# Performance work log

Hardware: AMD Instinct MI355X
Metric: run time of the kernel (lower is better)

## Reference

```python
import jax, jax.numpy as jnp
import numpy as np

B, T, V, D, U = 256, 1024, 6, 64, 64  # batch, seq, vocab, embed dim, lstm units


def _lstm_dir(x_seq, mask_seq, Wk, Wr, b, reverse):
    # x_seq: [B,T,D], mask_seq: [B,T] bool. Keras gate order: i, f, g(cell), o.
    Bc, Tc, _ = x_seq.shape
    Uc = Wr.shape[0]
    if reverse:
        x_seq = x_seq[:, ::-1, :]
        mask_seq = mask_seq[:, ::-1]
    # precompute input projections for all timesteps (one big GEMM)
    xproj = jnp.einsum('btd,dg->tbg', x_seq, Wk) + b          # [T,B,4U]
    m = jnp.swapaxes(mask_seq, 0, 1)[..., None]               # [T,B,1]

    def step(carry, inp):
        h, c = carry
        xp, mt = inp
        z = xp + h @ Wr                                        # [B,4U]
        i, f, g, o = jnp.split(z, 4, axis=-1)
        i = jax.nn.sigmoid(i)
        f = jax.nn.sigmoid(f)
        g = jnp.tanh(g)
        o = jax.nn.sigmoid(o)
        c_new = f * c + i * g
        h_new = o * jnp.tanh(c_new)
        # masked steps carry state through and repeat previous output
        h = jnp.where(mt, h_new, h)
        c = jnp.where(mt, c_new, c)
        return (h, c), h

    h0 = jnp.zeros((Bc, Uc), x_seq.dtype)
    _, ys = jax.lax.scan(step, (h0, h0), (xproj, m))           # ys: [T,B,U]
    ys = jnp.swapaxes(ys, 0, 1)                                # [B,T,U]
    if reverse:
        ys = ys[:, ::-1, :]
    return ys


def reference(tokens, emb, Wk_f, Wr_f, b_f, Wk_b, Wr_b, b_b, Wd, bd):
    x = emb[tokens]                                            # [B,T,D]
    mask = jnp.any(x != 0, axis=-1)                            # Masking(0): all-zero feature vec -> masked
    y_f = _lstm_dir(x, mask, Wk_f, Wr_f, b_f, reverse=False)   # [B,T,U]
    y_b = _lstm_dir(x, mask, Wk_b, Wr_b, b_b, reverse=True)    # [B,T,U]
    y = jnp.concatenate([y_f, y_b], axis=-1)                   # [B,T,2U]
    last = y[:, -1, :]                                         # [B,2U]
    return last @ Wd + bd                                      # [B,1]


def setup_inputs() -> dict:
    key = jax.random.key(0)
    ks = jax.random.split(key, 8)
    return {
        'tokens': jax.random.randint(ks[0], (B, T), 0, V, dtype=jnp.int32),
        'emb': jax.random.normal(ks[1], (V, D), dtype=jnp.float32),
        'Wk_f': jax.random.normal(ks[2], (D, 4 * U), dtype=jnp.float32) * 0.05,
        'Wr_f': jax.random.normal(ks[3], (U, 4 * U), dtype=jnp.float32) * 0.05,
        'b_f': jnp.zeros((4 * U,), dtype=jnp.float32),
        'Wk_b': jax.random.normal(ks[4], (D, 4 * U), dtype=jnp.float32) * 0.05,
        'Wr_b': jax.random.normal(ks[5], (U, 4 * U), dtype=jnp.float32) * 0.05,
        'b_b': jnp.zeros((4 * U,), dtype=jnp.float32),
        'Wd': jax.random.normal(ks[6], (2 * U, 1), dtype=jnp.float32) * 0.05,
        'bd': jnp.zeros((1,), dtype=jnp.float32),
    }
```

## Files before the change

kernel.cpp:

```cpp
#include <hip/hip_runtime.h>


constexpr int kB = 256;
constexpr int kT = 1024;
constexpr int kV = 6;
constexpr int kD = 64;
constexpr int kU = 64;
constexpr int kG = 256;

#define LOG2E 1.44269504f

typedef _Float16 v2h __attribute__((ext_vector_type(2)));

template <int CTRL>
__device__ __forceinline__ float dppf(float x) {
    return __int_as_float(
        __builtin_amdgcn_mov_dpp(__float_as_int(x), CTRL, 0xF, 0xF, true));
}
constexpr int kXor1 = 0xB1;
constexpr int kXor2 = 0x4E;
constexpr int kBc0 = 0x00, kBc1 = 0x55, kBc2 = 0xAA, kBc3 = 0xFF;

__device__ __forceinline__ float fast_rcp(float x) { return __builtin_amdgcn_rcpf(x); }
__device__ __forceinline__ float exp2_f(float x)   { return __builtin_amdgcn_exp2f(x); }
__device__ __forceinline__ float tanh_f(float z) { return 2.0f * fast_rcp(1.0f + exp2_f(-2.0f * LOG2E * z)) - 1.0f; }

__device__ __forceinline__ v2h as_v2h(float x) { return __builtin_bit_cast(v2h, x); }

__global__ __launch_bounds__(256)
__attribute__((amdgpu_waves_per_eu(1, 1)))
void bilstm_last_kernel(
    const int*   __restrict__ tokens,
    const float* __restrict__ emb,
    const float* __restrict__ Wk_f,
    const float* __restrict__ Wr_f,
    const float* __restrict__ b_f,
    const float* __restrict__ Wk_b,
    const float* __restrict__ b_b,
    const float* __restrict__ Wd,
    const float* __restrict__ bd,
    float*       __restrict__ out)
{
    __shared__ float s_emb[kV * kD];
    __shared__ int   __align__(16) s_tok[kT];
    __shared__ _Float16 __align__(16) s_hh[2][kU];
    __shared__ float s_red[4];

    const int b   = blockIdx.x;
    const int tid = threadIdx.x;
    const int l   = tid & 63;
    const int wv  = tid >> 6;
    const int s   = l & 3;
    const int k   = l >> 2;
    const int u   = wv * 16 + k;
    const int col = s * kU + u;

    for (int i = tid; i < kV * kD; i += 256) s_emb[i] = emb[i];
    ((int4*)s_tok)[tid] = ((const int4*)(tokens + b * kT))[tid];
    if (tid < 2 * kU) ((_Float16*)s_hh)[tid] = (_Float16)0.f;
    __syncthreads();

    unsigned int mbv = 0;
#pragma unroll
    for (int v = 0; v < kV; ++v) {
        const unsigned long long bb = __ballot(s_emb[v * kD + l] != 0.0f);
        mbv |= (bb != 0ull) ? (1u << v) : 0u;
    }
    const unsigned int smb = __builtin_amdgcn_readfirstlane(mbv);

    const int tokL = __builtin_amdgcn_readfirstlane(s_tok[kT - 1]);

    const bool  isg    = (s == 2);
    const float aScale = isg ? -2.0f * LOG2E : -LOG2E;
    const float aMul   = isg ? 2.0f : 1.0f;
    const float aAdd   = isg ? -1.0f : 0.0f;

    float pf0, pf1, pf2, pf3, pf4, pf5;
    float ab;
    {
        float afv[kV];
        const float bf = b_f[col];
#pragma unroll
        for (int v = 0; v < kV; ++v) afv[v] = bf;
        ab = b_b[col];
#pragma unroll 4
        for (int d = 0; d < kD; ++d) {
            const float wkf = Wk_f[d * kG + col];
            const float wkb = Wk_b[d * kG + col];
            afv[0] = fmaf(s_emb[0 * kD + d], wkf, afv[0]);
            afv[1] = fmaf(s_emb[1 * kD + d], wkf, afv[1]);
            afv[2] = fmaf(s_emb[2 * kD + d], wkf, afv[2]);
            afv[3] = fmaf(s_emb[3 * kD + d], wkf, afv[3]);
            afv[4] = fmaf(s_emb[4 * kD + d], wkf, afv[4]);
            afv[5] = fmaf(s_emb[5 * kD + d], wkf, afv[5]);
            ab     = fmaf(s_emb[tokL * kD + d], wkb, ab);
        }
        pf0 = afv[0]; pf1 = afv[1]; pf2 = afv[2];
        pf3 = afv[3]; pf4 = afv[4]; pf5 = afv[5];
    }
    auto sel6 = [&](int t) -> float {
        return t == 0 ? pf0 : t == 1 ? pf1 : t == 2 ? pf2
             : t == 3 ? pf3 : t == 4 ? pf4 : pf5;
    };

    float hb_val;
    {
        const float e = exp2_f(ab * aScale);
        const float r = fast_rcp(1.0f + e);
        const float a = fmaf(r, aMul, aAdd);
        const float cb = dppf<kBc0>(a) * dppf<kBc2>(a);
        const float hb = dppf<kBc3>(a) * tanh_f(cb);
        hb_val = ((smb >> tokL) & 1) ? hb : 0.0f;
    }

#define DECLH(g, p)                                                           \
    v2h wh##g##_##p;                                                          \
    wh##g##_##p.x = (_Float16)Wr_f[(16 * s + 2 * (p) + 0) * kG + ((g) * 64 + u)]; \
    wh##g##_##p.y = (_Float16)Wr_f[(16 * s + 2 * (p) + 1) * kG + ((g) * 64 + u)];
    DECLH(0,0) DECLH(0,1) DECLH(0,2) DECLH(0,3) DECLH(0,4) DECLH(0,5) DECLH(0,6) DECLH(0,7)
    DECLH(1,0) DECLH(1,1) DECLH(1,2) DECLH(1,3) DECLH(1,4) DECLH(1,5) DECLH(1,6) DECLH(1,7)
    DECLH(2,0) DECLH(2,1) DECLH(2,2) DECLH(2,3) DECLH(2,4) DECLH(2,5) DECLH(2,6) DECLH(2,7)
    DECLH(3,0) DECLH(3,1) DECLH(3,2) DECLH(3,3) DECLH(3,4) DECLH(3,5) DECLH(3,6) DECLH(3,7)
#undef DECLH

    float c = 0.0f, hreg = 0.0f;

    int st0 = __builtin_amdgcn_readfirstlane(s_tok[0]);
    int st1 = __builtin_amdgcn_readfirstlane(s_tok[1]);
    int st2 = __builtin_amdgcn_readfirstlane(s_tok[2]);
    int st3 = __builtin_amdgcn_readfirstlane(s_tok[3]);
    float zc0 = sel6(st0), zc1 = sel6(st1);
    int   mk0 = (smb >> st0) & 1, mk1 = (smb >> st1) & 1;

#define DOTG(g)                                                               \
        float pa##g = __builtin_amdgcn_fdot2(H0, wh##g##_0, 0.0f, false);     \
        float pb##g = __builtin_amdgcn_fdot2(H1, wh##g##_1, 0.0f, false);     \
        pa##g = __builtin_amdgcn_fdot2(H2, wh##g##_2, pa##g, false);          \
        pb##g = __builtin_amdgcn_fdot2(H3, wh##g##_3, pb##g, false);          \
        pa##g = __builtin_amdgcn_fdot2(H4, wh##g##_4, pa##g, false);          \
        pb##g = __builtin_amdgcn_fdot2(H5, wh##g##_5, pb##g, false);          \
        pa##g = __builtin_amdgcn_fdot2(H6, wh##g##_6, pa##g, false);          \
        pb##g = __builtin_amdgcn_fdot2(H7, wh##g##_7, pb##g, false);          \
        float p##g = pa##g + pb##g;

#define STEP(RP, WP, ZC, MK)                                                  \
    {                                                                         \
           \
        const float4* hp = (const float4*)s_hh[RP];                           \
        const float4 hv0 = hp[s * 2 + 0];                                     \
        const float4 hv1 = hp[s * 2 + 1];                                     \
        const v2h H0 = as_v2h(hv0.x), H1 = as_v2h(hv0.y);                     \
        const v2h H2 = as_v2h(hv0.z), H3 = as_v2h(hv0.w);                     \
        const v2h H4 = as_v2h(hv1.x), H5 = as_v2h(hv1.y);                     \
        const v2h H6 = as_v2h(hv1.z), H7 = as_v2h(hv1.w);                     \
        DOTG(0) DOTG(1) DOTG(2) DOTG(3)                                       \
            \
        p0 += dppf<kXor1>(p0); p1 += dppf<kXor1>(p1);                         \
        p2 += dppf<kXor1>(p2); p3 += dppf<kXor1>(p3);                         \
        float X = (s & 1) ? p1 : p0;                                          \
        float Y = (s & 1) ? p3 : p2;                                          \
        X += dppf<kXor2>(X); Y += dppf<kXor2>(Y);                             \
        const float z = ((s & 2) ? Y : X) + (ZC);                             \
                                      \
        const float e = exp2_f(z * aScale);                                   \
        const float r = fast_rcp(1.0f + e);                                   \
        const float a = fmaf(r, aMul, aAdd);                                  \
                     \
        const float ai = dppf<kBc0>(a);                                       \
        const float af = dppf<kBc1>(a);                                       \
        const float ag = dppf<kBc2>(a);                                       \
        const float ao = dppf<kBc3>(a);                                       \
        const float cn = fmaf(af, c, ai * ag);                                \
        const float hn = ao * tanh_f(cn);                                     \
        if (MK) { c = cn; hreg = hn; }                    \
        if (s == 0) s_hh[WP][u] = (_Float16)hreg;                             \
        __syncthreads();                                                      \
    }

#pragma unroll 1
    for (int t = 0; t < kT; t += 2) {
        STEP(0, 1, zc0, mk0)
        const int2 vt = *((const int2*)(s_tok + ((t + 4) & (kT - 1))));
        const float zn0 = sel6(st2); const int mn0 = (smb >> st2) & 1;
        const float zn1 = sel6(st3); const int mn1 = (smb >> st3) & 1;
        STEP(1, 0, zc1, mk1)
        st2 = __builtin_amdgcn_readfirstlane(vt.x);
        st3 = __builtin_amdgcn_readfirstlane(vt.y);
        zc0 = zn0; zc1 = zn1; mk0 = mn0; mk1 = mn1;
    }
#undef STEP
#undef DOTG

    {
        float v = (s == 0) ? (hreg * Wd[u] + hb_val * Wd[kU + u]) : 0.0f;
#pragma unroll
        for (int off = 32; off > 0; off >>= 1) v += __shfl_down(v, off, 64);
        if (l == 0) s_red[wv] = v;
    }
    __syncthreads();
    if (tid == 0) out[b] = (s_red[0] + s_red[1]) + (s_red[2] + s_red[3]) + bd[0];
}

extern "C" void kernel_launch(void* const* d_in, const int* in_sizes, int n_in,
                              void* d_out, int out_size, void* d_ws, size_t ws_size,
                              hipStream_t stream) {
    const int*   tokens = (const int*)d_in[0];
    const float* emb    = (const float*)d_in[1];
    const float* Wk_f   = (const float*)d_in[2];
    const float* Wr_f   = (const float*)d_in[3];
    const float* b_f    = (const float*)d_in[4];
    const float* Wk_b   = (const float*)d_in[5];
    const float* b_b    = (const float*)d_in[7];
    const float* Wd     = (const float*)d_in[8];
    const float* bd     = (const float*)d_in[9];
    float* out = (float*)d_out;

    bilstm_last_kernel<<<kB, 256, 0, stream>>>(
        tokens, emb, Wk_f, Wr_f, b_f, Wk_b, b_b, Wd, bd, out);
}
```

Measured before the change: 402.7 us.

## Pack two batch rows per block and move gate projections to shared memory

Each 512-thread block now processes two batch sequences, halving the grid to 128 blocks, with separate hidden-state buffers and token arrays per sequence. The six per-token input projections move from registers selected by a compare chain into a shared-memory table indexed by token, prefetched one step ahead. The aim is to use fewer blocks than the 256 CUs, so each CU's LDS and barrier traffic is shared across two sequences, and to free registers. In exchange, barriers now span 8 waves instead of 4, and a shared-memory load sits in each step.

```diff
diff --git a/kernel.cpp b/kernel.cpp
--- a/kernel.cpp
+++ b/kernel.cpp
@@ -27,9 +27,7 @@
 
 __device__ __forceinline__ v2h as_v2h(float x) { return __builtin_bit_cast(v2h, x); }
 
-__global__ __launch_bounds__(256)
-__attribute__((amdgpu_waves_per_eu(1, 1)))
-void bilstm_last_kernel(
+__global__ __launch_bounds__(512, 2) void bilstm_last_kernel(
     const int*   __restrict__ tokens,
     const float* __restrict__ emb,
     const float* __restrict__ Wk_f,
@@ -42,22 +40,26 @@
     float*       __restrict__ out)
 {
     __shared__ float s_emb[kV * kD];
-    __shared__ int   __align__(16) s_tok[kT];
-    __shared__ _Float16 __align__(16) s_hh[2][kU];
-    __shared__ float s_red[4];
-
-    const int b   = blockIdx.x;
+    __shared__ float __align__(16) s_projP[kV * kG];
+    __shared__ int   __align__(16) s_tok[2][kT];
+    __shared__ _Float16 __align__(16) s_hh[2][2][kU];
+    __shared__ float s_red[2][4];
+
+    const int b0  = blockIdx.x * 2;
     const int tid = threadIdx.x;
+    const int wv  = tid >> 6;
+    const int q   = wv >> 2;
+    const int w   = wv & 3;
     const int l   = tid & 63;
-    const int wv  = tid >> 6;
     const int s   = l & 3;
     const int k   = l >> 2;
-    const int u   = wv * 16 + k;
+    const int u   = w * 16 + k;
     const int col = s * kU + u;
-
-    for (int i = tid; i < kV * kD; i += 256) s_emb[i] = emb[i];
-    ((int4*)s_tok)[tid] = ((const int4*)(tokens + b * kT))[tid];
-    if (tid < 2 * kU) ((_Float16*)s_hh)[tid] = (_Float16)0.f;
+    const int idx = w * kU + l;
+
+    for (int i = tid; i < kV * kD; i += 512) s_emb[i] = emb[i];
+    ((int4*)s_tok)[tid] = ((const int4*)(tokens + b0 * kT))[tid];
+    if (tid < 2 * 2 * kU) ((_Float16*)s_hh)[tid] = (_Float16)0.f;
     __syncthreads();
 
     unsigned int mbv = 0;
@@ -68,14 +70,13 @@
     }
     const unsigned int smb = __builtin_amdgcn_readfirstlane(mbv);
 
-    const int tokL = __builtin_amdgcn_readfirstlane(s_tok[kT - 1]);
+    const int tokL = __builtin_amdgcn_readfirstlane(s_tok[q][kT - 1]);
 
     const bool  isg    = (s == 2);
     const float aScale = isg ? -2.0f * LOG2E : -LOG2E;
     const float aMul   = isg ? 2.0f : 1.0f;
     const float aAdd   = isg ? -1.0f : 0.0f;
 
-    float pf0, pf1, pf2, pf3, pf4, pf5;
     float ab;
     {
         float afv[kV];
@@ -95,13 +96,11 @@
             afv[5] = fmaf(s_emb[5 * kD + d], wkf, afv[5]);
             ab     = fmaf(s_emb[tokL * kD + d], wkb, ab);
         }
-        pf0 = afv[0]; pf1 = afv[1]; pf2 = afv[2];
-        pf3 = afv[3]; pf4 = afv[4]; pf5 = afv[5];
-    }
-    auto sel6 = [&](int t) -> float {
-        return t == 0 ? pf0 : t == 1 ? pf1 : t == 2 ? pf2
-             : t == 3 ? pf3 : t == 4 ? pf4 : pf5;
-    };
+        if (q == 0) {
+#pragma unroll
+            for (int v = 0; v < kV; ++v) s_projP[v * kG + idx] = afv[v];
+        }
+    }
 
     float hb_val;
     {
@@ -124,13 +123,12 @@
 #undef DECLH
 
     float c = 0.0f, hreg = 0.0f;
-
-    int st0 = __builtin_amdgcn_readfirstlane(s_tok[0]);
-    int st1 = __builtin_amdgcn_readfirstlane(s_tok[1]);
-    int st2 = __builtin_amdgcn_readfirstlane(s_tok[2]);
-    int st3 = __builtin_amdgcn_readfirstlane(s_tok[3]);
-    float zc0 = sel6(st0), zc1 = sel6(st1);
-    int   mk0 = (smb >> st0) & 1, mk1 = (smb >> st1) & 1;
+    __syncthreads();
+
+    int stok0 = __builtin_amdgcn_readfirstlane(s_tok[q][0]);
+    float zcur = s_projP[stok0 * kG + idx];
+    int   mskc = (smb >> stok0) & 1;
+    int   stokA = __builtin_amdgcn_readfirstlane(s_tok[q][1]);
 
 #define DOTG(g)                                                               \
         float pa##g = __builtin_amdgcn_fdot2(H0, wh##g##_0, 0.0f, false);     \
@@ -143,12 +141,16 @@
         pb##g = __builtin_amdgcn_fdot2(H7, wh##g##_7, pb##g, false);          \
         float p##g = pa##g + pb##g;
 
-#define STEP(RP, WP, ZC, MK)                                                  \
+#define STEP(RP, WP, TT)                                                      \
     {                                                                         \
-           \
-        const float4* hp = (const float4*)s_hh[RP];                           \
+                        \
+        const float4* hp = (const float4*)s_hh[RP][q];                        \
         const float4 hv0 = hp[s * 2 + 0];                                     \
         const float4 hv1 = hp[s * 2 + 1];                                     \
+                    \
+        const int   vtokB = s_tok[q][((TT) + 2) & (kT - 1)];                  \
+        const float znext = s_projP[stokA * kG + idx];                        \
+        const int   mskn  = (int)((smb >> stokA) & 1);                        \
         const v2h H0 = as_v2h(hv0.x), H1 = as_v2h(hv0.y);                     \
         const v2h H2 = as_v2h(hv0.z), H3 = as_v2h(hv0.w);                     \
         const v2h H4 = as_v2h(hv1.x), H5 = as_v2h(hv1.y);                     \
@@ -160,7 +162,7 @@
         float X = (s & 1) ? p1 : p0;                                          \
         float Y = (s & 1) ? p3 : p2;                                          \
         X += dppf<kXor2>(X); Y += dppf<kXor2>(Y);                             \
-        const float z = ((s & 2) ? Y : X) + (ZC);                             \
+        const float z = ((s & 2) ? Y : X) + zcur;                             \
                                       \
         const float e = exp2_f(z * aScale);                                   \
         const float r = fast_rcp(1.0f + e);                                   \
@@ -172,21 +174,17 @@
         const float ao = dppf<kBc3>(a);                                       \
         const float cn = fmaf(af, c, ai * ag);                                \
         const float hn = ao * tanh_f(cn);                                     \
-        if (MK) { c = cn; hreg = hn; }                    \
-        if (s == 0) s_hh[WP][u] = (_Float16)hreg;                             \
+        if (mskc) { c = cn; hreg = hn; }                  \
+        if (s == 0) s_hh[WP][q][u] = (_Float16)hreg;                          \
         __syncthreads();                                                      \
+        zcur = znext; mskc = mskn;                                            \
+        stokA = __builtin_amdgcn_readfirstlane(vtokB);                        \
     }
 
 #pragma unroll 1
     for (int t = 0; t < kT; t += 2) {
-        STEP(0, 1, zc0, mk0)
-        const int2 vt = *((const int2*)(s_tok + ((t + 4) & (kT - 1))));
-        const float zn0 = sel6(st2); const int mn0 = (smb >> st2) & 1;
-        const float zn1 = sel6(st3); const int mn1 = (smb >> st3) & 1;
-        STEP(1, 0, zc1, mk1)
-        st2 = __builtin_amdgcn_readfirstlane(vt.x);
-        st3 = __builtin_amdgcn_readfirstlane(vt.y);
-        zc0 = zn0; zc1 = zn1; mk0 = mn0; mk1 = mn1;
+        STEP(0, 1, t)
+        STEP(1, 0, t + 1)
     }
 #undef STEP
 #undef DOTG
@@ -195,10 +193,13 @@
         float v = (s == 0) ? (hreg * Wd[u] + hb_val * Wd[kU + u]) : 0.0f;
 #pragma unroll
         for (int off = 32; off > 0; off >>= 1) v += __shfl_down(v, off, 64);
-        if (l == 0) s_red[wv] = v;
+        if (l == 0) s_red[q][w] = v;
     }
     __syncthreads();
-    if (tid == 0) out[b] = (s_red[0] + s_red[1]) + (s_red[2] + s_red[3]) + bd[0];
+    if (tid == 0) {
+        out[b0]     = (s_red[0][0] + s_red[0][1]) + (s_red[0][2] + s_red[0][3]) + bd[0];
+        out[b0 + 1] = (s_red[1][0] + s_red[1][1]) + (s_red[1][2] + s_red[1][3]) + bd[0];
+    }
 }
 
 extern "C" void kernel_launch(void* const* d_in, const int* in_sizes, int n_in,
@@ -215,6 +216,6 @@
     const float* bd     = (const float*)d_in[9];
     float* out = (float*)d_out;
 
-    bilstm_last_kernel<<<kB, 256, 0, stream>>>(
+    bilstm_last_kernel<<<kB / 2, 512, 0, stream>>>(
         tokens, emb, Wk_f, Wr_f, b_f, Wk_b, b_b, Wd, bd, out);
 }
```

Measured after the change: 468.7 us. 1.16x slower.
